# Kernel tuning notes

Measured on AMD Instinct MI355X. Metric: run time of the kernel, lower is better.

## Reference

```python
import jax, jax.numpy as jnp
import numpy as np

PRE = 2000          # pre_wbf_detections
POST = 300          # post_wbf_detections
IOU_THRESH = 0.55   # wbf_iou_thresh
NUM_CLASSES = 5


def setup_inputs() -> dict:
    key = jax.random.key(0)
    k1, k2, k3, k4 = jax.random.split(key, 4)
    # realistic xyxy boxes in a 1024px image
    ctr = jax.random.uniform(k1, (PRE, 2), minval=0.0, maxval=1024.0)
    wh = jax.random.uniform(k2, (PRE, 2), minval=8.0, maxval=96.0)
    boxes = jnp.concatenate([ctr - wh / 2, ctr + wh / 2], axis=1)
    scores = jax.random.uniform(k3, (PRE, 1), minval=0.05, maxval=1.0)
    labels = jax.random.randint(k4, (PRE, 1), 0, NUM_CLASSES).astype(jnp.float32)
    x = jnp.concatenate([boxes, scores, labels], axis=1)  # (PRE, 6)
    return {"x": x}


def _iou_one_vs_many(box, mboxes):
    # torchvision-style box_iou of one box (4,) vs many (N,4)
    lt = jnp.maximum(box[:2], mboxes[:, :2])
    rb = jnp.minimum(box[2:], mboxes[:, 2:])
    wh = jnp.clip(rb - lt, 0.0)
    inter = wh[:, 0] * wh[:, 1]
    a1 = (box[2] - box[0]) * (box[3] - box[1])
    a2 = (mboxes[:, 2] - mboxes[:, 0]) * (mboxes[:, 3] - mboxes[:, 1])
    union = a1 + a2 - inter
    safe = jnp.where(union > 0, union, 1.0)
    return jnp.where(union > 0, inter / safe, 0.0)


def _wbf_forward(x):
    # Sequential WBF clustering. The torch code runs wbf() per unique class;
    # since a detection can only join a cluster of its own class and cluster
    # creation order within a class is preserved, a single sequential pass
    # with a class-equality check is mathematically identical (final result
    # is sorted by score, so per-class concatenation order is irrelevant).
    N = x.shape[0]
    # cluster state: score-weighted box sum, score sum, member count, class, valid
    init = (
        jnp.zeros((N, 4), x.dtype),   # sum of score*box per cluster
        jnp.zeros((N,), x.dtype),     # sum of scores per cluster
        jnp.zeros((N,), jnp.int32),   # member count per cluster
        jnp.zeros((N,), x.dtype),     # class id per cluster
        jnp.zeros((N,), bool),        # cluster slot valid
    )

    def step(carry, det):
        sum_wb, sum_s, cnt, cls, valid = carry
        box, score, c = det[:4], det[4], det[5]
        denom = jnp.where(valid, sum_s, 1.0)
        mboxes = sum_wb / denom[:, None]  # current merged boxes
        iou = _iou_one_vs_many(box, mboxes)
        match = valid & (cls == c) & (iou > IOU_THRESH)
        found = jnp.any(match)
        first = jnp.argmax(match)                  # first matching cluster
        n_valid = jnp.sum(valid).astype(jnp.int32)  # next free slot
        idx = jnp.where(found, first, n_valid)
        sum_wb = sum_wb.at[idx].add(score * box)
        sum_s = sum_s.at[idx].add(score)
        cnt = cnt.at[idx].add(1)
        cls = cls.at[idx].set(c)
        valid = valid.at[idx].set(True)
        return (sum_wb, sum_s, cnt, cls, valid), None

    (sum_wb, sum_s, cnt, cls, valid), _ = jax.lax.scan(step, init, x)

    denom = jnp.where(valid, sum_s, 1.0)
    boxes = sum_wb / denom[:, None]                              # weighted avg box
    scores = sum_s / jnp.maximum(cnt.astype(x.dtype), 1.0)       # mean score
    sort_key = jnp.where(valid, scores, -1.0)
    order = jnp.argsort(-sort_key)                               # descending by score
    top = order[:POST]
    vtop = valid[top]
    out = jnp.concatenate(
        [boxes[top], scores[top, None], cls[top, None]], axis=1)  # (POST, 6)
    return jnp.where(vtop[:, None], out, 0.0)


def reference(x):
    return _wbf_forward(x[:PRE])
```

## Files before the change

kernel.cpp:

```cpp
#include <hip/hip_runtime.h>

typedef unsigned long long u64;
typedef unsigned short u16;
typedef unsigned u32;
typedef unsigned char u8;

#define PRE   2000
#define POST  300
#define NCLS  5
#define CAP   512
#define INF   0x7fffffff

#define MID 0x1.19999A8p-1

template <int K> struct IC { static constexpr int v = K; };
template <int N, typename F> __device__ __forceinline__ void unrollN(F&& f) {
    if constexpr (N > 0) { unrollN<N - 1>(f); f(IC<N - 1>{}); }
}

__device__ __forceinline__ float rlF(float v, int l) {
    return __uint_as_float((u32)__builtin_amdgcn_readlane((int)__float_as_uint(v), l));
}

__device__ __forceinline__ bool iou_pred(float bx0, float bx1, float bx2, float bx3,
                                         float a1, float m0, float m1, float m2, float m3,
                                         float a2) {
    const float ltx = fmaxf(bx0, m0), lty = fmaxf(bx1, m1);
    const float rbx = fminf(bx2, m2), rby = fminf(bx3, m3);
    const float wd = fmaxf(rbx - ltx, 0.f), hg = fmaxf(rby - lty, 0.f);
    const float inter = wd * hg;
    const float uni = (a1 + a2) - inter;
    return (uni > 0.f) && ((double)inter >= MID * (double)uni);
}

__device__ __forceinline__ u64 mk_key(float sc, int g, int id) {
    return ~(((u64)__float_as_uint(sc) << 32) |
             ((u64)(unsigned)(0xFFFF - g) << 16) | (u64)id);
}

__global__ __launch_bounds__(512, 1) void wbf_matrix(const float* __restrict__ x,
                                                     u64* __restrict__ M,
                                                     float* __restrict__ dets,
                                                     int* __restrict__ nlist,
                                                     u64* __restrict__ keysg,
                                                     u32* __restrict__ histg) {
#pragma clang fp contract(off)
    __shared__ int s_wc[8];
    __shared__ u16 s_list[CAP];

    const int tid  = threadIdx.x;
    const int lane = tid & 63;
    const int wave = tid >> 6;
    const int b    = blockIdx.x;
    const int cls  = b >> 4;
    const float mycls = (float)cls;

    if (b == 1) for (int i = tid; i < NCLS * CAP; i += 512) keysg[i] = ~0ull;
    if (b == 2) for (int i = tid; i < 4096; i += 512) histg[i] = 0u;

    u64 wm[4]; int wcnt = 0;
    const int tb = wave * 256;
    #pragma unroll
    for (int i = 0; i < 4; ++i) {
        const int t = tb + i * 64 + lane;
        const bool pp = (t < PRE) && (x[t * 6 + 5] == mycls);
        wm[i] = __ballot(pp);
        wcnt += (int)__popcll(wm[i]);
    }
    if (lane == 0) s_wc[wave] = wcnt;
    __syncthreads();
    int off = 0, tot = 0;
    #pragma unroll
    for (int w = 0; w < 8; ++w) {
        const int cw = s_wc[w];
        off += (w < wave) ? cw : 0;
        tot += cw;
    }
    #pragma unroll
    for (int i = 0; i < 4; ++i) {
        const int t = tb + i * 64 + lane;
        const bool pp = ((wm[i] >> lane) & 1ull) != 0ull;
        const int pos = off + (int)__popcll(wm[i] & (((u64)1 << lane) - 1ull));
        if (pp && pos < CAP) s_list[pos] = (u16)t;
        off += (int)__popcll(wm[i]);
    }
    const int myn = (tot > CAP) ? CAP : tot;
    __syncthreads();

    {
        float qc0[8], qc1[8], qc2[8], qc3[8], ac[8];
        unrollN<8>([&](auto k_) {
            constexpr int K = decltype(k_)::v;
            const int c = K * 64 + lane;
            qc0[K] = 0.f; qc1[K] = 0.f; qc2[K] = 0.f; qc3[K] = 0.f; ac[K] = 0.f;
            if (c < myn) {
                const int g = s_list[c];
                const float* p = x + g * 6;
                const float b0 = p[0], b1 = p[1], b2 = p[2], b3 = p[3], sc = p[4];
                qc0[K] = (sc * b0) / sc; qc1[K] = (sc * b1) / sc;
                qc2[K] = (sc * b2) / sc; qc3[K] = (sc * b3) / sc;
                ac[K] = (qc2[K] - qc0[K]) * (qc3[K] - qc1[K]);
            }
        });
        const int slice = (b & 15) * 8 + wave;
        const int rlo = slice * 4;
        const int rhi = (rlo + 4 < myn) ? rlo + 4 : myn;
        const int nr = rhi - rlo;
        if (nr > 0) {
            float rv0 = 0.f, rv1 = 0.f, rv2 = 0.f, rv3 = 0.f;
            if (lane < nr) {
                const int g = s_list[rlo + lane];
                const float* p = x + g * 6;
                rv0 = p[0]; rv1 = p[1]; rv2 = p[2]; rv3 = p[3];
            }
            for (int i = 0; i < nr; ++i) {
                const int r = rlo + i;
                const float bx0 = rlF(rv0, i), bx1 = rlF(rv1, i);
                const float bx2 = rlF(rv2, i), bx3 = rlF(rv3, i);
                const float a1 = (bx2 - bx0) * (bx3 - bx1);
                const int Wmax = r >> 6;
                unrollN<8>([&](auto w_) {
                    constexpr int W = decltype(w_)::v;
                    if (W <= Wmax) {
                        const int c = W * 64 + lane;
                        const bool pred = (c < r) &&
                            iou_pred(bx0, bx1, bx2, bx3, a1, qc0[W], qc1[W], qc2[W], qc3[W], ac[W]);
                        const u64 bits = __ballot(pred);
                        if (lane == 0) M[((size_t)(cls * CAP + r)) * 8 + W] = bits;
                    }
                });
            }
        }
    }

    if ((b & 15) == 0) {
        for (int rr = tid; rr < myn; rr += 512) {
            const int g = s_list[rr];
            const float* p = x + g * 6;
            const float b0 = p[0], b1 = p[1], b2 = p[2], b3 = p[3], sc = p[4];
            float* dr = dets + (size_t)(cls * CAP + rr) * 8;
            dr[0] = b0; dr[1] = b1; dr[2] = b2; dr[3] = b3;
            dr[4] = sc; dr[5] = (b2 - b0) * (b3 - b1);
            ((int*)dr)[6] = g; ((int*)dr)[7] = 0;
        }
        if (tid == 0) nlist[cls] = myn;
    }
}

__global__ __launch_bounds__(512, 1) void wbf_scan(const u64* __restrict__ M,
                                                   const float* __restrict__ dets,
                                                   const int* __restrict__ nlist,
                                                   float* __restrict__ recs,
                                                   int* __restrict__ cnts,
                                                   u64* __restrict__ keysg,
                                                   u32* __restrict__ histg) {
#pragma clang fp contract(off)
    __shared__ __align__(16) char s_buf[57408];
    u8*  s_mtx = (u8*)s_buf;
    float (*s_det)[8]  = (float (*)[8])(s_buf + 32768);
    float (*s_dov)[16] = (float (*)[16])(s_buf + 49152);
    u8*  s_ab          = (u8*)(s_buf + 57344);

    const int tid  = threadIdx.x;
    const int lane = tid & 63;
    const int wave = tid >> 6;
    const int cls  = blockIdx.x;

    const int myn = nlist[cls];

    {
        const ulonglong2* Mg = (const ulonglong2*)(M + (size_t)cls * CAP * 8);
        ulonglong2* Ml = (ulonglong2*)s_mtx;
        const int nit = myn * 4;
        for (int it = tid; it < nit; it += 512) Ml[it] = Mg[it];
    }
    {
        const float4* Dg = (const float4*)(dets + (size_t)cls * CAP * 8);
        float4* Dl = (float4*)s_det;
        const int nit = myn * 2;
        for (int it = tid; it < nit; it += 512) Dl[it] = Dg[it];
    }
    if (tid < 64) s_ab[tid] = 0;
    __syncthreads();
    if (wave != 0) return;

    u32 aliveB = 0;
    int dirtyCnt = 0;
    bool consA = false;
    int resCode = 0, resIdx = 0;
    float dR0 = 0.f, dR1 = 0.f, dR2 = 0.f, dR3 = 0.f, dRa = 0.f;
    float dS0 = 0.f, dS1 = 0.f, dS2 = 0.f, dS3 = 0.f, dSs = 0.f;
    int dRank = INF, dGi = 0, dCnt = 0;
    float rm0 = 0.f, rm1 = 0.f, rm2 = 0.f, rm3 = 0.f, rma = 0.f;

    auto resolve = [&](int r, float bx0, float bx1, float bx2, float bx3,
                       float sc, float a1, u32 rowByte, u64 balC) {
        const u32 mC = rowByte & aliveB;
        int rank_c = INF;
        if (balC) {
            const int wl = (int)__builtin_ctzll(balC);
            const u32 byte = (u32)__builtin_amdgcn_readlane((int)mC, wl);
            rank_c = wl * 8 + (int)__builtin_ctz(byte);
        }
        const int rcs = (rank_c == INF) ? 0 : rank_c;
        const float4 cbv = *(const float4*)&s_det[rcs][0];
        const float4 cbe = *(const float4*)&s_det[rcs][4];
        const float cb0 = cbv.x, cb1 = cbv.y, cb2 = cbv.z, cb3 = cbv.w;
        const float csc = cbe.x;
        const int cgi = __float_as_int(cbe.z);

        int rank_d = INF, di = -1;
        if (dirtyCnt > 0) {
            const int DN = (dirtyCnt < 64) ? dirtyCnt : 64;
            const bool p = (lane < DN) &&
                iou_pred(bx0, bx1, bx2, bx3, a1, dR0, dR1, dR2, dR3, dRa);
            const int myrk = p ? dRank : INF;
            u64 mk = __ballot(p);
            while (mk) {
                const int l = (int)__builtin_ctzll(mk);
                mk &= mk - 1;
                const int rk = __builtin_amdgcn_readlane(myrk, l);
                if (rk < rank_d) { rank_d = rk; di = l; }
            }
            const int DH2 = (dirtyCnt < 128) ? dirtyCnt : 128;
            for (int dd = 64; dd < DH2; ++dd) {
                const float* dv = s_dov[dd];
                if (iou_pred(bx0, bx1, bx2, bx3, a1, dv[0], dv[1], dv[2], dv[3], dv[4])) {
                    const int rk = ((const int*)dv)[10];
                    if (rk < rank_d) { rank_d = rk; di = dd; }
                }
            }
        }
        if (rank_c == INF && rank_d == INF) {
            aliveB |= ((r >> 3) == lane) ? (1u << (r & 7)) : 0u;
            resCode = 0;
        } else if (rank_c < rank_d) {
            const int rc = rank_c;
            aliveB &= ~(((rc >> 3) == lane) ? (1u << (rc & 7)) : 0u);
            const float ns0 = (csc * cb0) + sc * bx0;
            const float ns1 = (csc * cb1) + sc * bx1;
            const float ns2 = (csc * cb2) + sc * bx2;
            const float ns3 = (csc * cb3) + sc * bx3;
            const float nss = csc + sc;
            const float nm0 = ns0 / nss, nm1 = ns1 / nss;
            const float nm2 = ns2 / nss, nm3 = ns3 / nss;
            const float nar = (nm2 - nm0) * (nm3 - nm1);
            const int D = dirtyCnt;
            if (D < 64) {
                if (lane == D) {
                    dR0 = nm0; dR1 = nm1; dR2 = nm2; dR3 = nm3; dRa = nar;
                    dS0 = ns0; dS1 = ns1; dS2 = ns2; dS3 = ns3; dSs = nss;
                    dRank = rc; dGi = cgi; dCnt = 2;
                }
            } else if (D < 128) {
                if (lane == 0) {
                    float* dv = s_dov[D];
                    dv[0] = nm0; dv[1] = nm1; dv[2] = nm2; dv[3] = nm3; dv[4] = nar;
                    dv[5] = ns0; dv[6] = ns1; dv[7] = ns2; dv[8] = ns3; dv[9] = nss;
                    ((int*)dv)[10] = rc; ((int*)dv)[11] = cgi; ((int*)dv)[12] = 2;
                }
            }
            dirtyCnt++;
            resCode = 1; resIdx = D;
            rm0 = nm0; rm1 = nm1; rm2 = nm2; rm3 = nm3; rma = nar;
        } else {
            float f0, f1, f2, f3, fs; int nct;
            if (di < 64) {
                f0 = rlF(dS0, di) + sc * bx0; f1 = rlF(dS1, di) + sc * bx1;
                f2 = rlF(dS2, di) + sc * bx2; f3 = rlF(dS3, di) + sc * bx3;
                fs = rlF(dSs, di) + sc;
                nct = __builtin_amdgcn_readlane(dCnt, di) + 1;
            } else {
                const float* dv = s_dov[di];
                f0 = dv[5] + sc * bx0; f1 = dv[6] + sc * bx1;
                f2 = dv[7] + sc * bx2; f3 = dv[8] + sc * bx3;
                fs = dv[9] + sc;
                nct = ((const int*)dv)[12] + 1;
            }
            const float nm0 = f0 / fs, nm1 = f1 / fs, nm2 = f2 / fs, nm3 = f3 / fs;
            const float nar = (nm2 - nm0) * (nm3 - nm1);
            if (di < 64) {
                if (lane == di) {
                    dR0 = nm0; dR1 = nm1; dR2 = nm2; dR3 = nm3; dRa = nar;
                    dS0 = f0; dS1 = f1; dS2 = f2; dS3 = f3; dSs = fs; dCnt = nct;
                }
            } else {
                if (lane == 0) {
                    float* dw = s_dov[di];
                    dw[0] = nm0; dw[1] = nm1; dw[2] = nm2; dw[3] = nm3; dw[4] = nar;
                    dw[5] = f0; dw[6] = f1; dw[7] = f2; dw[8] = f3; dw[9] = fs;
                    ((int*)dw)[12] = nct;
                }
            }
            rm0 = nm0; rm1 = nm1; rm2 = nm2; rm3 = nm3; rma = nar;
            resCode = 2; resIdx = di;
        }
    };

    unrollN<8>([&](auto k_) {
        constexpr int K = decltype(k_)::v;
        const int r0 = K * 64;
        if (r0 < myn) {
            const int cnt = (myn - r0 < 64) ? (myn - r0) : 64;
            const bool valid = lane < cnt;
            const u64 validM = (cnt == 64) ? ~0ull : (((u64)1 << cnt) - 1ull);
            u64 orv = 0ull;
            {
                const int rr = r0 + (valid ? lane : 0);
                const u64* rp = (const u64*)&s_mtx[(size_t)rr * 64];
                const u64* av = (const u64*)s_ab;
                unrollN<8>([&](auto w_) {
                    constexpr int W = decltype(w_)::v;
                    if (W < K)       orv |= rp[W] & av[W];
                    else if (W == K) orv |= rp[W];
                });
            }
            const u64 rowW = __ballot(valid && orv != 0ull);
            float4 db = make_float4(0.f, 0.f, 0.f, 0.f);
            float2 de = make_float2(1.f, 0.f);
            if (valid) {
                db = *(const float4*)&s_det[r0 + lane][0];
                de = *(const float2*)&s_det[r0 + lane][4];
            }
            u64 dmaskLo = 0ull, dmaskHi = 0ull;
            if (!consA) {
                const int DN = (dirtyCnt < 64) ? dirtyCnt : 64;
                for (int d = 0; d < DN; ++d) {
                    const float m0 = rlF(dR0, d), m1 = rlF(dR1, d);
                    const float m2 = rlF(dR2, d), m3 = rlF(dR3, d);
                    const float ma = rlF(dRa, d);
                    const bool pp = valid && iou_pred(db.x, db.y, db.z, db.w, de.y,
                                                     m0, m1, m2, m3, ma);
                    if (pp) dmaskLo |= 1ull << d;
                }
                const int DH = (dirtyCnt < 128) ? dirtyCnt : 128;
                for (int dd = 64; dd < DH; ++dd) {
                    const float* dv = s_dov[dd];
                    const bool pp = valid && iou_pred(db.x, db.y, db.z, db.w, de.y,
                                                     dv[0], dv[1], dv[2], dv[3], dv[4]);
                    if (pp) dmaskHi |= 1ull << (dd - 64);
                }
            }
            u64 danyb = __ballot((dmaskLo | dmaskHi) != 0ull);

            u32 prB[8]; int prP[8];
            {
                u64 t = consA ? validM : ((danyb | rowW) & validM);
                #pragma unroll
                for (int i = 0; i < 8; ++i) {
                    const int f = t ? (int)__builtin_ctzll(t) : 0;
                    prP[i] = t ? f : 64;
                    prB[i] = (u32)s_mtx[(size_t)(r0 + f) * 64 + lane];
                    t &= t - 1ull;
                }
            }

            int p = 0;
            while (p < cnt) {
                u64 vm = consA ? validM : ((danyb | rowW) & validM);
                vm &= ~(((u64)1 << p) - 1ull);
                const int F = vm ? (int)__builtin_ctzll(vm) : cnt;
                {
                    const int lo = r0 + p, h2 = r0 + F;
                    int s = lo - 8 * lane; s = (s > 0) ? s : 0;
                    int e = h2 - 8 * lane; e = (e < 8) ? e : 8;
                    if (e > s) aliveB |= ((0xFFu >> (8 - (e - s))) << s);
                }
                s_ab[lane] = (u8)aliveB;
                if (F >= cnt) break;
                const int r = r0 + F;
                u32 rowByte = 0u; bool hit = false;
                #pragma unroll
                for (int i = 0; i < 8; ++i)
                    if (prP[i] == F) { rowByte = prB[i]; hit = true; }
                if (!hit) rowByte = (u32)s_mtx[(size_t)r * 64 + lane];
                const u64 balCq = __ballot((rowByte & aliveB) != 0u);
                const bool Fdirty = consA || (((danyb >> F) & 1ull) != 0ull);
                if (!Fdirty && balCq == 0ull) {
                    aliveB |= ((r >> 3) == lane) ? (1u << (r & 7)) : 0u;
                    s_ab[lane] = (u8)aliveB;
                } else {
                    const float bx0 = rlF(db.x, F), bx1 = rlF(db.y, F);
                    const float bx2 = rlF(db.z, F), bx3 = rlF(db.w, F);
                    const float sc = rlF(de.x, F), a1 = rlF(de.y, F);
                    resolve(r, bx0, bx1, bx2, bx3, sc, a1, rowByte, balCq);
                    s_ab[lane] = (u8)aliveB;
                    if (resCode != 0) {
                        const int idx = resIdx;
                        if (idx < 128) {
                            const bool pnew = valid && (lane > F) &&
                                iou_pred(db.x, db.y, db.z, db.w, de.y,
                                         rm0, rm1, rm2, rm3, rma);
                            const u64 nb = __ballot(pnew);
                            const u64 bit = (nb >> lane) & 1ull;
                            if (idx < 64)
                                dmaskLo = (dmaskLo & ~(1ull << idx)) | (bit << idx);
                            else
                                dmaskHi = (dmaskHi & ~(1ull << (idx - 64))) | (bit << (idx - 64));
                            danyb = __ballot((dmaskLo | dmaskHi) != 0ull);
                        } else {
                            consA = true;
                        }
                    }
                }
                p = F + 1;
            }
        }
    });

    int wo = 0;
    for (int Kw = 0; Kw < 8; ++Kw) {
        u64 am = 0ull;
        #pragma unroll
        for (int bb = 0; bb < 8; ++bb)
            am |= (u64)(u32)(u8)__builtin_amdgcn_readlane((int)aliveB, Kw * 8 + bb) << (8 * bb);
        const int j = Kw * 64 + lane;
        const bool pred = (am >> lane) & 1ull;
        if (pred) {
            const int pos = wo + (int)__popcll(am & (((u64)1 << lane) - 1));
            const float b0 = s_det[j][0], b1 = s_det[j][1];
            const float b2 = s_det[j][2], b3 = s_det[j][3];
            const float sc = s_det[j][4];
            const int g = ((const int*)s_det[j])[6];
            const int id = cls * CAP + pos;
            float* rec = recs + (size_t)id * 8;
            rec[0] = (sc * b0) / sc; rec[1] = (sc * b1) / sc;
            rec[2] = (sc * b2) / sc; rec[3] = (sc * b3) / sc;
            rec[4] = sc;
            ((int*)rec)[5] = g;
            const u64 skey = mk_key(sc, g, id);
            keysg[id] = skey;
            atomicAdd(&histg[(u32)(skey >> 52)], 1u);
        }
        wo += (int)__popcll(am);
    }
    const int demit = (dirtyCnt < 128) ? dirtyCnt : 128;
    {
        const int dreg = (demit < 64) ? demit : 64;
        if (lane < dreg) {
            const int id = cls * CAP + wo + lane;
            float* rec = recs + (size_t)id * 8;
            const float scd = dSs / (float)dCnt;
            rec[0] = dR0; rec[1] = dR1; rec[2] = dR2; rec[3] = dR3;
            rec[4] = scd;
            ((int*)rec)[5] = dGi;
            const u64 skey = mk_key(scd, dGi, id);
            keysg[id] = skey;
            atomicAdd(&histg[(u32)(skey >> 52)], 1u);
        }
        for (int d = 64 + lane; d < demit; d += 64) {
            const float* dv = s_dov[d];
            const int id = cls * CAP + wo + d;
            float* rec = recs + (size_t)id * 8;
            const float scd = dv[9] / (float)(((const int*)dv)[12]);
            const int g = ((const int*)dv)[11];
            rec[0] = dv[0]; rec[1] = dv[1]; rec[2] = dv[2]; rec[3] = dv[3];
            rec[4] = scd;
            ((int*)rec)[5] = g;
            const u64 skey = mk_key(scd, g, id);
            keysg[id] = skey;
            atomicAdd(&histg[(u32)(skey >> 52)], 1u);
        }
    }
    if (lane == 0) cnts[cls] = wo + demit;
}

__global__ __launch_bounds__(512, 1) void wbf_sort(const u64* __restrict__ keysg,
                                                   const u32* __restrict__ histg,
                                                   const float* __restrict__ recs,
                                                   const int* __restrict__ cnts,
                                                   float* __restrict__ out) {
    __shared__ __align__(16) char s_buf[28864];
    u64* keysL  = (u64*)s_buf;
    u64* cand   = (u64*)(s_buf + 20480);
    u64* sorted = (u64*)(s_buf + 24576);
    u32* part   = (u32*)(s_buf + 28672);
    int* scal   = (int*)(s_buf + 28704);

    const int tid  = threadIdx.x;
    const int lane = tid & 63;
    const int wave = tid >> 6;

    if (tid == 0) { scal[0] = 0; scal[1] = 0; scal[2] = 0; }

    int n = 0;
    #pragma unroll
    for (int w = 0; w < NCLS; ++w) n += cnts[w];
    const int target = (POST < n) ? POST : n;

    u32 p = 0;
    #pragma unroll
    for (int k = 0; k < 8; ++k) p += histg[tid * 8 + k];
    u32 v = p;
    #pragma unroll
    for (int o2 = 1; o2 < 64; o2 <<= 1) {
        const u32 t = (u32)__shfl_up((int)v, o2);
        if (lane >= o2) v += t;
    }
    if (lane == 63) part[wave] = v;
    __syncthreads();
    u32 base = 0;
    #pragma unroll
    for (int w = 0; w < 8; ++w) base += (w < wave) ? part[w] : 0u;
    const u32 I = base + v;
    const u32 E = I - p;
    if ((int)E < target && (int)I >= target) { scal[0] = tid; scal[1] = (int)E; }
    __syncthreads();
    const int T = scal[0];
    int cum = scal[1];
    int B = T * 8 + 7;
    for (int bb = T * 8; bb < T * 8 + 8; ++bb) {
        const int h = (int)histg[bb];
        if (cum + h >= target) { B = bb; break; }
        cum += h;
    }
    const int candCount = cum + (int)histg[B];

    if (candCount <= 512) {
        #pragma unroll
        for (int b2 = 0; b2 < NCLS * CAP; b2 += 512) {
            const u64 kk = keysg[b2 + tid];
            const bool pred = ((u32)(kk >> 52) <= (u32)B);
            const u64 m = __ballot(pred);
            if (m) {
                int wbase = 0;
                if (lane == 0) wbase = atomicAdd(&scal[2], (int)__popcll(m));
                wbase = __builtin_amdgcn_readfirstlane(wbase);
                if (pred) {
                    const int pos = wbase + (int)__popcll(m & (((u64)1 << lane) - 1ull));
                    cand[pos] = kk;
                }
            }
        }
        __syncthreads();
        if (tid >= candCount) cand[tid] = (~0ull << 16) | (u64)(0xF000u + tid);
        __syncthreads();
        const u64 myk = cand[tid];
        int rk = 0;
        #pragma unroll 4
        for (int j = 0; j < 512; ++j) {
            const u64 kj = cand[j];
            rk += (int)(kj < myk);
        }
        sorted[rk] = myk;
        __syncthreads();
    } else {
        for (int i = tid; i < NCLS * CAP; i += 512) keysL[i] = keysg[i];
        __syncthreads();
        u64 myk5[5]; int rk5[5];
        #pragma unroll
        for (int s = 0; s < 5; ++s) { myk5[s] = keysL[s * 512 + tid]; rk5[s] = 0; }
        for (int j = 0; j < NCLS * CAP; ++j) {
            const u64 kj = keysL[j];
            #pragma unroll
            for (int s = 0; s < 5; ++s)
                rk5[s] += (int)((kj < myk5[s]) || (kj == myk5[s] && j < s * 512 + tid));
        }
        #pragma unroll
        for (int s = 0; s < 5; ++s)
            if (rk5[s] < 512) sorted[rk5[s]] = myk5[s];
        __syncthreads();
    }

    if (tid < POST) {
        float* o = out + tid * 6;
        if (tid < target) {
            const u64 key = ~sorted[tid];
            const int id = (int)(key & 0xFFFFull);
            const float* rec = recs + (size_t)id * 8;
            o[0] = rec[0]; o[1] = rec[1]; o[2] = rec[2]; o[3] = rec[3];
            o[4] = __uint_as_float((unsigned)(key >> 32));
            o[5] = (float)(id >> 9);
        } else {
            o[0] = 0.f; o[1] = 0.f; o[2] = 0.f; o[3] = 0.f; o[4] = 0.f; o[5] = 0.f;
        }
    }
}

extern "C" void kernel_launch(void* const* d_in, const int* in_sizes, int n_in,
                              void* d_out, int out_size, void* d_ws, size_t ws_size,
                              hipStream_t stream) {
    const float* x = (const float*)d_in[0];
    float* out = (float*)d_out;
    u64*   M     = (u64*)d_ws;
    float* dets  = (float*)((char*)d_ws + 163840);
    float* recs  = (float*)((char*)d_ws + 245760);
    int*   cnts  = (int*)((char*)d_ws + 327680);
    int*   nlist = cnts + 16;
    u64*   keysg = (u64*)((char*)d_ws + 327936);
    u32*   histg = (u32*)((char*)d_ws + 348416);
    wbf_matrix<<<NCLS * 16, 512, 0, stream>>>(x, M, dets, nlist, keysg, histg);
    wbf_scan<<<NCLS, 512, 0, stream>>>(M, dets, nlist, recs, cnts, keysg, histg);
    wbf_sort<<<1, 512, 0, stream>>>(keysg, histg, recs, cnts, out);
}
```

Before: 97.08 us.

## Fuse matrix, scan and sort kernels into one persistent kernel with spin-wait sync

The three kernel launches are merged into a single 81-block kernel. Blocks coordinate through global atomic counters: a magic flag marks that buffers have been initialised, per-class counters mark that the IoU matrix rows are complete, and a finish counter releases a dedicated sort block. Per-class detection records are now built directly in the scan block's shared memory instead of being staged through global memory. This removes two launch gaps and one global round-trip. In exchange it depends on all blocks being co-resident for the spin-waits. The magic flag is never cleared between calls, so a stale flag or counter from a previous call could let blocks run ahead of re-initialisation.

```diff
diff --git a/kernel.cpp b/kernel.cpp
--- a/kernel.cpp
+++ b/kernel.cpp
@@ -10,12 +10,19 @@
 #define NCLS  5
 #define CAP   512
 #define INF   0x7fffffff
+#define MAGIC 0x13579BDFu
+#define NBLK  81
+#define SORTB 80
 
 #define MID 0x1.19999A8p-1
 
 template <int K> struct IC { static constexpr int v = K; };
 template <int N, typename F> __device__ __forceinline__ void unrollN(F&& f) {
     if constexpr (N > 0) { unrollN<N - 1>(f); f(IC<N - 1>{}); }
+}
+
+__device__ __forceinline__ u32 aload_acq(u32* p) {
+    return __hip_atomic_load(p, __ATOMIC_ACQUIRE, __HIP_MEMORY_SCOPE_AGENT);
 }
 
 __device__ __forceinline__ float rlF(float v, int l) {
@@ -38,25 +45,156 @@
              ((u64)(unsigned)(0xFFFF - g) << 16) | (u64)id);
 }
 
-__global__ __launch_bounds__(512, 1) void wbf_matrix(const float* __restrict__ x,
-                                                     u64* __restrict__ M,
-                                                     float* __restrict__ dets,
-                                                     int* __restrict__ nlist,
-                                                     u64* __restrict__ keysg,
-                                                     u32* __restrict__ histg) {
+__global__ __launch_bounds__(512, 1) void wbf_all(const float* __restrict__ x,
+                                                  u64* __restrict__ M,
+                                                  float* __restrict__ recs,
+                                                  int* __restrict__ cnts,
+                                                  u64* __restrict__ keysg,
+                                                  u32* __restrict__ histg,
+                                                  u32* __restrict__ ctrl,
+                                                  float* __restrict__ out) {
 #pragma clang fp contract(off)
-    __shared__ int s_wc[8];
-    __shared__ u16 s_list[CAP];
+    __shared__ __align__(16) char s_buf[58464];
+    u8*  s_mtx = (u8*)s_buf;
+    float (*s_det)[8]  = (float (*)[8])(s_buf + 32768);
+    float (*s_dov)[16] = (float (*)[16])(s_buf + 49152);
+    u8*  s_ab          = (u8*)(s_buf + 57344);
+    u16* s_list        = (u16*)(s_buf + 57408);
+    int* s_wc          = (int*)(s_buf + 58432);
 
     const int tid  = threadIdx.x;
     const int lane = tid & 63;
     const int wave = tid >> 6;
     const int b    = blockIdx.x;
-    const int cls  = b >> 4;
+
+    if (b == SORTB) {
+        u64* keysL  = (u64*)s_buf;
+        u64* cand   = (u64*)(s_buf + 20480);
+        u64* sorted = (u64*)(s_buf + 24576);
+        u32* part   = (u32*)(s_buf + 28672);
+        int* scal   = (int*)(s_buf + 28704);
+
+        if (tid == 0) { while (aload_acq(&ctrl[32]) != MAGIC) {} }
+        __syncthreads();
+        if (tid == 0) { while (aload_acq(&ctrl[16]) < (u32)NCLS) {} }
+        __syncthreads();
+        if (tid == 0) { scal[0] = 0; scal[1] = 0; scal[2] = 0; }
+
+        int n = 0;
+        #pragma unroll
+        for (int w = 0; w < NCLS; ++w) n += cnts[w];
+        const int target = (POST < n) ? POST : n;
+
+        u32 p = 0;
+        #pragma unroll
+        for (int k = 0; k < 8; ++k) p += histg[tid * 8 + k];
+        u32 v = p;
+        #pragma unroll
+        for (int o2 = 1; o2 < 64; o2 <<= 1) {
+            const u32 t = (u32)__shfl_up((int)v, o2);
+            if (lane >= o2) v += t;
+        }
+        if (lane == 63) part[wave] = v;
+        __syncthreads();
+        u32 base = 0;
+        #pragma unroll
+        for (int w = 0; w < 8; ++w) base += (w < wave) ? part[w] : 0u;
+        const u32 I = base + v;
+        const u32 E = I - p;
+        if ((int)E < target && (int)I >= target) { scal[0] = tid; scal[1] = (int)E; }
+        __syncthreads();
+        const int T = scal[0];
+        int cum = scal[1];
+        int B = T * 8 + 7;
+        for (int bb = T * 8; bb < T * 8 + 8; ++bb) {
+            const int h = (int)histg[bb];
+            if (cum + h >= target) { B = bb; break; }
+            cum += h;
+        }
+        const int candCount = cum + (int)histg[B];
+
+        if (candCount <= 512) {
+            #pragma unroll
+            for (int b2 = 0; b2 < NCLS * CAP; b2 += 512) {
+                const u64 kk = keysg[b2 + tid];
+                const bool pred = ((u32)(kk >> 52) <= (u32)B);
+                const u64 m = __ballot(pred);
+                if (m) {
+                    int wbase = 0;
+                    if (lane == 0) wbase = atomicAdd(&scal[2], (int)__popcll(m));
+                    wbase = __builtin_amdgcn_readfirstlane(wbase);
+                    if (pred) {
+                        const int pos = wbase + (int)__popcll(m & (((u64)1 << lane) - 1ull));
+                        cand[pos] = kk;
+                    }
+                }
+            }
+            __syncthreads();
+            if (tid >= candCount) cand[tid] = (~0ull << 16) | (u64)(0xF000u + tid);
+            __syncthreads();
+            const u64 myk = cand[tid];
+            int rk = 0;
+            #pragma unroll 4
+            for (int j = 0; j < 512; ++j) {
+                const u64 kj = cand[j];
+                rk += (int)(kj < myk);
+            }
+            sorted[rk] = myk;
+            __syncthreads();
+        } else {
+            for (int i = tid; i < NCLS * CAP; i += 512) keysL[i] = keysg[i];
+            __syncthreads();
+            u64 myk5[5]; int rk5[5];
+            #pragma unroll
+            for (int s = 0; s < 5; ++s) { myk5[s] = keysL[s * 512 + tid]; rk5[s] = 0; }
+            for (int j = 0; j < NCLS * CAP; ++j) {
+                const u64 kj = keysL[j];
+                #pragma unroll
+                for (int s = 0; s < 5; ++s)
+                    rk5[s] += (int)((kj < myk5[s]) || (kj == myk5[s] && j < s * 512 + tid));
+            }
+            #pragma unroll
+            for (int s = 0; s < 5; ++s)
+                if (rk5[s] < 512) sorted[rk5[s]] = myk5[s];
+            __syncthreads();
+        }
+
+        if (tid < POST) {
+            float* o = out + tid * 6;
+            if (tid < target) {
+                const u64 key = ~sorted[tid];
+                const int id = (int)(key & 0xFFFFull);
+                const float* rec = recs + (size_t)id * 8;
+                o[0] = rec[0]; o[1] = rec[1]; o[2] = rec[2]; o[3] = rec[3];
+                o[4] = __uint_as_float((unsigned)(key >> 32));
+                o[5] = (float)(id >> 9);
+            } else {
+                o[0] = 0.f; o[1] = 0.f; o[2] = 0.f; o[3] = 0.f; o[4] = 0.f; o[5] = 0.f;
+            }
+        }
+        return;
+    }
+
+    const int cls = b >> 4;
     const float mycls = (float)cls;
 
-    if (b == 1) for (int i = tid; i < NCLS * CAP; i += 512) keysg[i] = ~0ull;
-    if (b == 2) for (int i = tid; i < 4096; i += 512) histg[i] = 0u;
+    if (b == 0) {
+        for (int i = tid; i < NCLS * CAP; i += 512) keysg[i] = ~0ull;
+        for (int i = tid; i < 4096; i += 512) histg[i] = 0u;
+        if (tid == 0) {
+            for (int i = 0; i < NCLS; ++i)
+                __hip_atomic_store(&ctrl[i], 0u, __ATOMIC_RELAXED, __HIP_MEMORY_SCOPE_AGENT);
+            __hip_atomic_store(&ctrl[16], 0u, __ATOMIC_RELAXED, __HIP_MEMORY_SCOPE_AGENT);
+        }
+        __syncthreads();
+        if (tid == 0) {
+            __threadfence();
+            __hip_atomic_store(&ctrl[32], MAGIC, __ATOMIC_RELEASE, __HIP_MEMORY_SCOPE_AGENT);
+        }
+    } else {
+        if (tid == 0) { while (aload_acq(&ctrl[32]) != MAGIC) {} }
+    }
+    __syncthreads();
 
     u64 wm[4]; int wcnt = 0;
     const int tb = wave * 256;
@@ -132,55 +270,29 @@
             }
         }
     }
-
-    if ((b & 15) == 0) {
-        for (int rr = tid; rr < myn; rr += 512) {
-            const int g = s_list[rr];
-            const float* p = x + g * 6;
-            const float b0 = p[0], b1 = p[1], b2 = p[2], b3 = p[3], sc = p[4];
-            float* dr = dets + (size_t)(cls * CAP + rr) * 8;
-            dr[0] = b0; dr[1] = b1; dr[2] = b2; dr[3] = b3;
-            dr[4] = sc; dr[5] = (b2 - b0) * (b3 - b1);
-            ((int*)dr)[6] = g; ((int*)dr)[7] = 0;
-        }
-        if (tid == 0) nlist[cls] = myn;
-    }
-}
-
-__global__ __launch_bounds__(512, 1) void wbf_scan(const u64* __restrict__ M,
-                                                   const float* __restrict__ dets,
-                                                   const int* __restrict__ nlist,
-                                                   float* __restrict__ recs,
-                                                   int* __restrict__ cnts,
-                                                   u64* __restrict__ keysg,
-                                                   u32* __restrict__ histg) {
-#pragma clang fp contract(off)
-    __shared__ __align__(16) char s_buf[57408];
-    u8*  s_mtx = (u8*)s_buf;
-    float (*s_det)[8]  = (float (*)[8])(s_buf + 32768);
-    float (*s_dov)[16] = (float (*)[16])(s_buf + 49152);
-    u8*  s_ab          = (u8*)(s_buf + 57344);
-
-    const int tid  = threadIdx.x;
-    const int lane = tid & 63;
-    const int wave = tid >> 6;
-    const int cls  = blockIdx.x;
-
-    const int myn = nlist[cls];
-
+    __threadfence();
+    if (lane == 0)
+        __hip_atomic_fetch_add(&ctrl[cls], 1u, __ATOMIC_RELEASE, __HIP_MEMORY_SCOPE_AGENT);
+
+    if ((b & 15) != 0) return;
+
+    for (int rr = tid; rr < myn; rr += 512) {
+        const int g = s_list[rr];
+        const float* p = x + g * 6;
+        const float b0 = p[0], b1 = p[1], b2 = p[2], b3 = p[3], sc = p[4];
+        s_det[rr][0] = b0; s_det[rr][1] = b1; s_det[rr][2] = b2; s_det[rr][3] = b3;
+        s_det[rr][4] = sc; s_det[rr][5] = (b2 - b0) * (b3 - b1);
+        ((int*)s_det[rr])[6] = g;
+    }
+    if (tid < 64) s_ab[tid] = 0;
+    if (tid == 0) { while (aload_acq(&ctrl[cls]) < 128u) {} }
+    __syncthreads();
     {
         const ulonglong2* Mg = (const ulonglong2*)(M + (size_t)cls * CAP * 8);
         ulonglong2* Ml = (ulonglong2*)s_mtx;
         const int nit = myn * 4;
         for (int it = tid; it < nit; it += 512) Ml[it] = Mg[it];
     }
-    {
-        const float4* Dg = (const float4*)(dets + (size_t)cls * CAP * 8);
-        float4* Dl = (float4*)s_det;
-        const int nit = myn * 2;
-        for (int it = tid; it < nit; it += 512) Dl[it] = Dg[it];
-    }
-    if (tid < 64) s_ab[tid] = 0;
     __syncthreads();
     if (wave != 0) return;
 
@@ -463,118 +575,9 @@
         }
     }
     if (lane == 0) cnts[cls] = wo + demit;
-}
-
-__global__ __launch_bounds__(512, 1) void wbf_sort(const u64* __restrict__ keysg,
-                                                   const u32* __restrict__ histg,
-                                                   const float* __restrict__ recs,
-                                                   const int* __restrict__ cnts,
-                                                   float* __restrict__ out) {
-    __shared__ __align__(16) char s_buf[28864];
-    u64* keysL  = (u64*)s_buf;
-    u64* cand   = (u64*)(s_buf + 20480);
-    u64* sorted = (u64*)(s_buf + 24576);
-    u32* part   = (u32*)(s_buf + 28672);
-    int* scal   = (int*)(s_buf + 28704);
-
-    const int tid  = threadIdx.x;
-    const int lane = tid & 63;
-    const int wave = tid >> 6;
-
-    if (tid == 0) { scal[0] = 0; scal[1] = 0; scal[2] = 0; }
-
-    int n = 0;
-    #pragma unroll
-    for (int w = 0; w < NCLS; ++w) n += cnts[w];
-    const int target = (POST < n) ? POST : n;
-
-    u32 p = 0;
-    #pragma unroll
-    for (int k = 0; k < 8; ++k) p += histg[tid * 8 + k];
-    u32 v = p;
-    #pragma unroll
-    for (int o2 = 1; o2 < 64; o2 <<= 1) {
-        const u32 t = (u32)__shfl_up((int)v, o2);
-        if (lane >= o2) v += t;
-    }
-    if (lane == 63) part[wave] = v;
-    __syncthreads();
-    u32 base = 0;
-    #pragma unroll
-    for (int w = 0; w < 8; ++w) base += (w < wave) ? part[w] : 0u;
-    const u32 I = base + v;
-    const u32 E = I - p;
-    if ((int)E < target && (int)I >= target) { scal[0] = tid; scal[1] = (int)E; }
-    __syncthreads();
-    const int T = scal[0];
-    int cum = scal[1];
-    int B = T * 8 + 7;
-    for (int bb = T * 8; bb < T * 8 + 8; ++bb) {
-        const int h = (int)histg[bb];
-        if (cum + h >= target) { B = bb; break; }
-        cum += h;
-    }
-    const int candCount = cum + (int)histg[B];
-
-    if (candCount <= 512) {
-        #pragma unroll
-        for (int b2 = 0; b2 < NCLS * CAP; b2 += 512) {
-            const u64 kk = keysg[b2 + tid];
-            const bool pred = ((u32)(kk >> 52) <= (u32)B);
-            const u64 m = __ballot(pred);
-            if (m) {
-                int wbase = 0;
-                if (lane == 0) wbase = atomicAdd(&scal[2], (int)__popcll(m));
-                wbase = __builtin_amdgcn_readfirstlane(wbase);
-                if (pred) {
-                    const int pos = wbase + (int)__popcll(m & (((u64)1 << lane) - 1ull));
-                    cand[pos] = kk;
-                }
-            }
-        }
-        __syncthreads();
-        if (tid >= candCount) cand[tid] = (~0ull << 16) | (u64)(0xF000u + tid);
-        __syncthreads();
-        const u64 myk = cand[tid];
-        int rk = 0;
-        #pragma unroll 4
-        for (int j = 0; j < 512; ++j) {
-            const u64 kj = cand[j];
-            rk += (int)(kj < myk);
-        }
-        sorted[rk] = myk;
-        __syncthreads();
-    } else {
-        for (int i = tid; i < NCLS * CAP; i += 512) keysL[i] = keysg[i];
-        __syncthreads();
-        u64 myk5[5]; int rk5[5];
-        #pragma unroll
-        for (int s = 0; s < 5; ++s) { myk5[s] = keysL[s * 512 + tid]; rk5[s] = 0; }
-        for (int j = 0; j < NCLS * CAP; ++j) {
-            const u64 kj = keysL[j];
-            #pragma unroll
-            for (int s = 0; s < 5; ++s)
-                rk5[s] += (int)((kj < myk5[s]) || (kj == myk5[s] && j < s * 512 + tid));
-        }
-        #pragma unroll
-        for (int s = 0; s < 5; ++s)
-            if (rk5[s] < 512) sorted[rk5[s]] = myk5[s];
-        __syncthreads();
-    }
-
-    if (tid < POST) {
-        float* o = out + tid * 6;
-        if (tid < target) {
-            const u64 key = ~sorted[tid];
-            const int id = (int)(key & 0xFFFFull);
-            const float* rec = recs + (size_t)id * 8;
-            o[0] = rec[0]; o[1] = rec[1]; o[2] = rec[2]; o[3] = rec[3];
-            o[4] = __uint_as_float((unsigned)(key >> 32));
-            o[5] = (float)(id >> 9);
-        } else {
-            o[0] = 0.f; o[1] = 0.f; o[2] = 0.f; o[3] = 0.f; o[4] = 0.f; o[5] = 0.f;
-        }
-    }
+    __threadfence();
+    if (lane == 0)
+        __hip_atomic_fetch_add(&ctrl[16], 1u, __ATOMIC_RELEASE, __HIP_MEMORY_SCOPE_AGENT);
 }
 
 extern "C" void kernel_launch(void* const* d_in, const int* in_sizes, int n_in,
@@ -583,13 +586,10 @@
     const float* x = (const float*)d_in[0];
     float* out = (float*)d_out;
     u64*   M     = (u64*)d_ws;
-    float* dets  = (float*)((char*)d_ws + 163840);
-    float* recs  = (float*)((char*)d_ws + 245760);
-    int*   cnts  = (int*)((char*)d_ws + 327680);
-    int*   nlist = cnts + 16;
-    u64*   keysg = (u64*)((char*)d_ws + 327936);
-    u32*   histg = (u32*)((char*)d_ws + 348416);
-    wbf_matrix<<<NCLS * 16, 512, 0, stream>>>(x, M, dets, nlist, keysg, histg);
-    wbf_scan<<<NCLS, 512, 0, stream>>>(M, dets, nlist, recs, cnts, keysg, histg);
-    wbf_sort<<<1, 512, 0, stream>>>(keysg, histg, recs, cnts, out);
-}
+    float* recs  = (float*)((char*)d_ws + 163840);
+    int*   cnts  = (int*)((char*)d_ws + 245760);
+    u64*   keysg = (u64*)((char*)d_ws + 246016);
+    u32*   histg = (u32*)((char*)d_ws + 266496);
+    u32*   ctrl  = (u32*)((char*)d_ws + 282880);
+    wbf_all<<<NBLK, 512, 0, stream>>>(x, M, recs, cnts, keysg, histg, ctrl, out);
+}
```

After: 113.8 us. 1.17x slower.

## Split final rank sort across eight blocks with deterministic candidate compaction

Applied to the files above, without the earlier changes.

The final top-K sort kernel now launches eight blocks. In the common path each block ranks a 64-key slice of the candidates: every wave counts against one 64-key chunk, and the partial counts are summed in shared memory before writing directly to the output at the computed rank. Candidate compaction now uses per-wave counts and barriers instead of a shared-memory atomic, so every block builds the same ordering. Each block still redoes the histogram prefix and compaction, and the overflow path runs only in block 0. The intent is to cut the serial 512-iteration rank loop per thread down to 64 iterations.

```diff
diff --git a/kernel.cpp b/kernel.cpp
--- a/kernel.cpp
+++ b/kernel.cpp
@@ -10,6 +10,7 @@
 #define NCLS  5
 #define CAP   512
 #define INF   0x7fffffff
+#define SORTG 8
 
 #define MID 0x1.19999A8p-1
 
@@ -471,17 +472,19 @@
                                                    const int* __restrict__ cnts,
                                                    float* __restrict__ out) {
     __shared__ __align__(16) char s_buf[28864];
-    u64* keysL  = (u64*)s_buf;
-    u64* cand   = (u64*)(s_buf + 20480);
-    u64* sorted = (u64*)(s_buf + 24576);
-    u32* part   = (u32*)(s_buf + 28672);
-    int* scal   = (int*)(s_buf + 28704);
+    u64* keysL   = (u64*)s_buf;
+    u64* cand    = (u64*)(s_buf + 20480);
+    u32* partial = (u32*)(s_buf + 24576);
+    u32* part    = (u32*)(s_buf + 26624);
+    int* wcnt    = (int*)(s_buf + 26656);
+    int* scal    = (int*)(s_buf + 26688);
 
     const int tid  = threadIdx.x;
     const int lane = tid & 63;
     const int wave = tid >> 6;
-
-    if (tid == 0) { scal[0] = 0; scal[1] = 0; scal[2] = 0; }
+    const int g    = blockIdx.x;
+
+    if (tid == 0) { scal[0] = 0; scal[1] = 0; }
 
     int n = 0;
     #pragma unroll
@@ -517,34 +520,56 @@
     const int candCount = cum + (int)histg[B];
 
     if (candCount <= 512) {
+        int running = 0;
         #pragma unroll
-        for (int b2 = 0; b2 < NCLS * CAP; b2 += 512) {
-            const u64 kk = keysg[b2 + tid];
+        for (int c5 = 0; c5 < 5; ++c5) {
+            const u64 kk = keysg[c5 * 512 + tid];
             const bool pred = ((u32)(kk >> 52) <= (u32)B);
             const u64 m = __ballot(pred);
-            if (m) {
-                int wbase = 0;
-                if (lane == 0) wbase = atomicAdd(&scal[2], (int)__popcll(m));
-                wbase = __builtin_amdgcn_readfirstlane(wbase);
-                if (pred) {
-                    const int pos = wbase + (int)__popcll(m & (((u64)1 << lane) - 1ull));
-                    cand[pos] = kk;
-                }
-            }
-        }
-        __syncthreads();
+            if (lane == 0) wcnt[wave] = (int)__popcll(m);
+            __syncthreads();
+            int wb = running;
+            #pragma unroll
+            for (int w = 0; w < 8; ++w) {
+                wb += (w < wave) ? wcnt[w] : 0;
+                running += wcnt[w];
+            }
+            if (pred)
+                cand[wb + (int)__popcll(m & (((u64)1 << lane) - 1ull))] = kk;
+            __syncthreads();
+        }
         if (tid >= candCount) cand[tid] = (~0ull << 16) | (u64)(0xF000u + tid);
         __syncthreads();
-        const u64 myk = cand[tid];
-        int rk = 0;
-        #pragma unroll 4
-        for (int j = 0; j < 512; ++j) {
-            const u64 kj = cand[j];
-            rk += (int)(kj < myk);
-        }
-        sorted[rk] = myk;
+
+        const u64 kc = cand[g * 64 + lane];
+        int pc = 0;
+        #pragma unroll 8
+        for (int j = 0; j < 64; ++j) {
+            const u64 kj = cand[wave * 64 + j];
+            pc += (int)(kj < kc);
+        }
+        partial[wave * 64 + lane] = (u32)pc;
         __syncthreads();
+        if (wave == 0) {
+            int rk = 0;
+            #pragma unroll
+            for (int w = 0; w < 8; ++w) rk += (int)partial[w * 64 + lane];
+            if (rk < target) {
+                const u64 key = ~kc;
+                const int id = (int)(key & 0xFFFFull);
+                const float* rec = recs + (size_t)id * 8;
+                float* o = out + rk * 6;
+                o[0] = rec[0]; o[1] = rec[1]; o[2] = rec[2]; o[3] = rec[3];
+                o[4] = __uint_as_float((unsigned)(key >> 32));
+                o[5] = (float)(id >> 9);
+            }
+        }
+        if (g == 0 && tid >= target && tid < POST) {
+            float* o = out + tid * 6;
+            o[0] = 0.f; o[1] = 0.f; o[2] = 0.f; o[3] = 0.f; o[4] = 0.f; o[5] = 0.f;
+        }
     } else {
+        if (g != 0) return;
         for (int i = tid; i < NCLS * CAP; i += 512) keysL[i] = keysg[i];
         __syncthreads();
         u64 myk5[5]; int rk5[5];
@@ -557,21 +582,20 @@
                 rk5[s] += (int)((kj < myk5[s]) || (kj == myk5[s] && j < s * 512 + tid));
         }
         #pragma unroll
-        for (int s = 0; s < 5; ++s)
-            if (rk5[s] < 512) sorted[rk5[s]] = myk5[s];
-        __syncthreads();
-    }
-
-    if (tid < POST) {
-        float* o = out + tid * 6;
-        if (tid < target) {
-            const u64 key = ~sorted[tid];
-            const int id = (int)(key & 0xFFFFull);
-            const float* rec = recs + (size_t)id * 8;
-            o[0] = rec[0]; o[1] = rec[1]; o[2] = rec[2]; o[3] = rec[3];
-            o[4] = __uint_as_float((unsigned)(key >> 32));
-            o[5] = (float)(id >> 9);
-        } else {
+        for (int s = 0; s < 5; ++s) {
+            const int rk = rk5[s];
+            if (rk < target) {
+                const u64 key = ~myk5[s];
+                const int id = (int)(key & 0xFFFFull);
+                const float* rec = recs + (size_t)id * 8;
+                float* o = out + rk * 6;
+                o[0] = rec[0]; o[1] = rec[1]; o[2] = rec[2]; o[3] = rec[3];
+                o[4] = __uint_as_float((unsigned)(key >> 32));
+                o[5] = (float)(id >> 9);
+            }
+        }
+        if (tid >= target && tid < POST) {
+            float* o = out + tid * 6;
             o[0] = 0.f; o[1] = 0.f; o[2] = 0.f; o[3] = 0.f; o[4] = 0.f; o[5] = 0.f;
         }
     }
@@ -591,5 +615,5 @@
     u32*   histg = (u32*)((char*)d_ws + 348416);
     wbf_matrix<<<NCLS * 16, 512, 0, stream>>>(x, M, dets, nlist, keysg, histg);
     wbf_scan<<<NCLS, 512, 0, stream>>>(M, dets, nlist, recs, cnts, keysg, histg);
-    wbf_sort<<<1, 512, 0, stream>>>(keysg, histg, recs, cnts, out);
-}
+    wbf_sort<<<SORTG, 512, 0, stream>>>(keysg, histg, recs, cnts, out);
+}
```

New measurement: 90.75 us (median of 2 runs). 6.5% less time.
